# Performance work log

Hardware: AMD Instinct MI355X
Metric: run time of the kernel (lower is better)

## Reference

```python
import jax, jax.numpy as jnp
import numpy as np
import math

THRESHOLD = 0.9
CAPACITY_FACTOR = 1.0
ALPHA = 0.01


def setup_inputs() -> dict:
    key = jax.random.key(0)
    k1, k2 = jax.random.split(key)
    B, T, H, E = 8, 4096, 1024, 64
    x = jax.random.normal(k1, (B, T, H), dtype=jnp.float32)
    # kaiming-uniform-ish gate init: bound = 1/sqrt(H)
    gate_w = jax.random.uniform(k2, (E, H), dtype=jnp.float32,
                                minval=-1.0 / math.sqrt(H), maxval=1.0 / math.sqrt(H))
    return {"x": x, "gate_w": gate_w}


def reference(x, gate_w):
    B, T, H = x.shape
    E = gate_w.shape[0]
    N = B * T
    x_flat = x.reshape(N, H)

    logits = x_flat @ gate_w.T                      # [N, E]
    probs = jax.nn.softmax(logits, axis=-1)

    # per-token descending sort of expert probs
    idx_sorted = jnp.argsort(-probs, axis=-1)       # [N, E]
    p_sorted = jnp.take_along_axis(probs, idx_sorted, axis=-1)

    # variable-k threshold selection on cumulative prob
    csum = jnp.cumsum(p_sorted, axis=-1)
    reached = csum >= THRESHOLD
    reached = reached.at[:, -1].set(True)
    k_idx = jnp.argmax(reached, axis=-1)            # first True per row
    arangeE = jnp.arange(E)[None, :]
    assign_sorted = arangeE <= k_idx[:, None]       # prefix-select in sorted order

    # scatter back to expert order via inverse permutation
    inv_perm = jnp.argsort(idx_sorted, axis=-1)
    assign_mask = jnp.take_along_axis(assign_sorted, inv_perm, axis=-1)

    # priority score R: prob minus rank, -1e9 for unassigned
    rank = jnp.arange(1, E + 1, dtype=probs.dtype)[None, :]
    R_sorted = jnp.where(assign_sorted, p_sorted - rank, jnp.float32(-1e9))
    R = jnp.take_along_axis(R_sorted, inv_perm, axis=-1)  # [N, E]

    # capacity-based dropping: keep top-C tokens per expert column
    capacity = int(math.ceil(N / E) * CAPACITY_FACTOR)
    C = min(capacity, N)
    tok_sorted = jnp.argsort(-R, axis=0)            # [N, E]
    topC_tok = tok_sorted[:C, :]                    # [C, E]
    cols = jnp.broadcast_to(jnp.arange(E)[None, :], topC_tok.shape)
    keep_flags = jnp.zeros((N, E), dtype=bool).at[topC_tok, cols].set(True)

    final_mask = assign_mask & keep_flags
    scores_sel = jnp.where(final_mask, probs, jnp.zeros_like(probs))

    # aux load-balance loss on top-1 assignments
    top1_idx = jnp.argmax(probs, axis=-1)
    top1_scores = jnp.max(probs, axis=-1)
    fi = jnp.mean(jax.nn.one_hot(top1_idx, E, dtype=probs.dtype), axis=0)
    pi = jax.ops.segment_sum(top1_scores, top1_idx, num_segments=E) / jnp.float32(N)
    aux_loss = E * jnp.sum(fi * pi) * ALPHA

    return final_mask, scores_sel, aux_loss, top1_idx
```

## Files before the change

### kernel.cpp

```cpp
#include <hip/hip_runtime.h>
#include <math.h>

#define NTOK 32768
#define HDIM 1024
#define NEXP 64
#define NE   (NTOK * NEXP)
#define CAP  512
#define TB   64
#define CK   64
#define XRS  68
#define CAND 6144
#define QMAX 2048

__device__ __forceinline__ unsigned f2key(float f) {
  unsigned u = __float_as_uint(f);
  return (u & 0x80000000u) ? ~u : (u | 0x80000000u);
}
__device__ __forceinline__ int bin_of(unsigned k) {
  if (k & 0x80000000u) return 0;
  float f = __uint_as_float(~k);
  f = fminf(f, 64.5f);
  return (int)f;
}

__global__ void init_kernel(unsigned* cnt, float* sumP, unsigned* ghist) {
  int i = blockIdx.x * 256 + threadIdx.x;
  if (i < NEXP) { cnt[i] = 0u; sumP[i] = 0.f; }
  if (i < NEXP * NEXP) ghist[i] = 0u;
}

__global__ __launch_bounds__(512) void router_kernel(
    const float* __restrict__ x, const float* __restrict__ w,
    float* __restrict__ probs, unsigned* __restrict__ keyNE,
    unsigned* __restrict__ keyEN, unsigned long long* __restrict__ assignB,
    unsigned* __restrict__ cnt, float* __restrict__ sumP,
    unsigned* __restrict__ ghist, float* __restrict__ out) {
  __shared__ float sm[(TB + NEXP) * XRS];
  __shared__ unsigned lhist[NEXP * 65];
  const int tid  = threadIdx.x;
  const int wid  = tid >> 6, lane = tid & 63;
  const int tokv = wid >> 1, expv = wid & 1;
  const int tg   = lane >> 3, eg = lane & 7;
  const int t0   = blockIdx.x * TB;
  float* xs  = sm;
  float* wsm = sm + TB * XRS;

  for (int i = tid; i < NEXP * 65; i += 512) lhist[i] = 0u;

  float acc[2][4] = {};

  for (int hc = 0; hc < HDIM / CK; ++hc) {
    const int h0 = hc * CK;
#pragma unroll
    for (int r = 0; r < 2; ++r) {
      int idx = tid + r * 512;
      int row = idx >> 4, c4 = idx & 15;
      *(float4*)(xs + row * XRS + c4 * 4) =
          *(const float4*)(x + (size_t)(t0 + row) * HDIM + h0 + c4 * 4);
      *(float4*)(wsm + row * XRS + c4 * 4) =
          *(const float4*)(w + (size_t)row * HDIM + h0 + c4 * 4);
    }
    __syncthreads();
#pragma unroll
    for (int s = 0; s < 16; ++s) {
      const int k4 = s * 4;
      float4 xv0 = *(const float4*)(xs + (tokv * 16 + tg) * XRS + k4);
      float4 xv1 = *(const float4*)(xs + (tokv * 16 + 8 + tg) * XRS + k4);
#pragma unroll
      for (int j = 0; j < 4; ++j) {
        float4 wv = *(const float4*)(wsm + (expv * 32 + j * 8 + eg) * XRS + k4);
        acc[0][j] += xv0.x * wv.x + xv0.y * wv.y + xv0.z * wv.z + xv0.w * wv.w;
        acc[1][j] += xv1.x * wv.x + xv1.y * wv.y + xv1.z * wv.z + xv1.w * wv.w;
      }
    }
    __syncthreads();
  }

  float* ls = sm;
  unsigned* kt = (unsigned*)(sm + TB * 65);
#pragma unroll
  for (int i = 0; i < 2; ++i) {
    int tl = tokv * 16 + i * 8 + tg;
#pragma unroll
    for (int j = 0; j < 4; ++j)
      ls[tl * 65 + expv * 32 + j * 8 + eg] = acc[i][j];
  }
  __syncthreads();

  for (int i = 0; i < 8; ++i) {
    const int tl = wid * 8 + i;
    const int t  = t0 + tl;
    float l = ls[tl * 65 + lane];
    float mx = l;
#pragma unroll
    for (int m = 32; m >= 1; m >>= 1) mx = fmaxf(mx, __shfl_xor(mx, m));
    float ex = expf(l - mx);
    float ssum = ex;
#pragma unroll
    for (int m = 32; m >= 1; m >>= 1) ssum += __shfl_xor(ssum, m);
    float p = ex / ssum;
    int rank = 0; float csum = p;
#pragma unroll
    for (int d = 1; d < 64; ++d) {
      float pj = __shfl_xor(p, d);
      int H = d; H |= H >> 1; H |= H >> 2; H |= H >> 4; H -= (H >> 1);
      bool jlt = (lane & H) != 0;
      bool gt = (pj > p) || (pj == p && jlt);
      rank += gt ? 1 : 0;
      csum += gt ? pj : 0.f;
    }
    int kc = (csum >= 0.9f) ? rank : 63;
#pragma unroll
    for (int m = 32; m >= 1; m >>= 1) kc = min(kc, __shfl_xor(kc, m));
    const bool assign = (rank <= kc);
    float R = assign ? (p - (float)(rank + 1)) : -1e9f;
    unsigned key = f2key(R);
    probs[(size_t)t * NEXP + lane] = p;
    keyNE[(size_t)t * NEXP + lane] = key;
    kt[tl * 65 + lane] = key;
    atomicAdd(&lhist[lane * 65 + bin_of(key)], 1u);
    unsigned long long ab = __ballot(assign);
    if (lane == 0) assignB[t] = ab;
    if (rank == 0) {
      out[(size_t)2 * NE + 1 + t] = (float)lane;
      atomicAdd(&cnt[lane], 1u);
      atomicAdd(&sumP[lane], p);
    }
  }
  __syncthreads();
#pragma unroll
  for (int r = 0; r < 8; ++r) {
    int idx = tid + r * 512;
    int e = idx >> 6, tl = idx & 63;
    keyEN[(size_t)e * NTOK + t0 + tl] = kt[tl * 65 + e];
  }
  for (int idx = tid; idx < NEXP * NEXP; idx += 512) {
    int ee = idx >> 6, b = idx & 63;
    unsigned v = lhist[ee * 65 + b];
    if (v) atomicAdd(&ghist[idx], v);
  }
}

__global__ __launch_bounds__(1024) void select_kernel(
    const unsigned* __restrict__ keyEN, const unsigned* __restrict__ ghist,
    unsigned* __restrict__ theta, int* __restrict__ tieCut) {
  const int e = blockIdx.x;
  const unsigned* col = keyEN + (size_t)e * NTOK;
  const int tid = threadIdx.x, wid = tid >> 6;
  __shared__ unsigned wh[16][256];
  __shared__ unsigned h[256];
  __shared__ unsigned cA_k[CAND], cA_t[CAND], cB_k[CAND], cB_t[CAND];
  __shared__ unsigned s_n, s_b;
  __shared__ int s_rb, s_need, s_cnt;
  __shared__ unsigned s_theta; __shared__ int s_cut;

  if (tid == 0) {
    unsigned run = 0; int rb = -1, need = 0, cc = 0;
    for (int r = 0; r < 64; ++r) {
      unsigned c = ghist[e * 64 + r];
      if (rb < 0 && run + c >= CAP) { rb = r; need = CAP - (int)run; cc = (int)c; }
      run += c;
    }
    s_rb = rb; s_need = need; s_cnt = cc;
  }
  __syncthreads();
  if (s_rb < 0) {
    if (tid == 0) { theta[e] = f2key(-1e9f); tieCut[e] = -1; }
    return;
  }
  const int rb = s_rb;
  int need = s_need, cnt = s_cnt;
  unsigned pmask = 0u, pval = 0u;
  int level = 0;

  while (cnt > CAND && level < 4) {
    const int sh = 24 - 8 * level;
    for (int r = tid; r < 16 * 256; r += 1024) ((unsigned*)wh)[r] = 0u;
    __syncthreads();
    for (int t = tid; t < NTOK; t += 1024) {
      unsigned k = col[t];
      if (bin_of(k) == rb && (k & pmask) == pval)
        atomicAdd(&wh[wid][(k >> sh) & 255u], 1u);
    }
    __syncthreads();
    if (tid < 256) {
      unsigned s = 0;
      for (int wv = 0; wv < 16; ++wv) s += wh[wv][tid];
      h[tid] = s;
    }
    __syncthreads();
    if (tid == 0) {
      unsigned cum = 0;
      for (int d = 255; d >= 0; --d) {
        if (cum + h[d] >= (unsigned)need) {
          s_b = (unsigned)d; s_need = need - (int)cum; s_cnt = (int)h[d];
          break;
        }
        cum += h[d];
      }
    }
    __syncthreads();
    need = s_need; cnt = s_cnt;
    pmask |= (255u << sh); pval |= (s_b << sh);
    level++;
    __syncthreads();
  }

  if (cnt > CAND) {
    int lo = 0, hi = NTOK - 1;
    while (lo < hi) {
      int mid = (lo + hi) >> 1;
      if (tid == 0) s_n = 0u;
      __syncthreads();
      for (int t = tid; t <= mid; t += 1024)
        if (col[t] == pval) atomicAdd(&s_n, 1u);
      __syncthreads();
      if ((int)s_n >= need) hi = mid; else lo = mid + 1;
      __syncthreads();
    }
    if (tid == 0) { theta[e] = pval; tieCut[e] = lo; }
    return;
  }

  if (tid == 0) s_n = 0u;
  __syncthreads();
  for (int t = tid; t < NTOK; t += 1024) {
    unsigned k = col[t];
    if (bin_of(k) == rb && (k & pmask) == pval) {
      unsigned i = atomicAdd(&s_n, 1u);
      cA_k[i] = k; cA_t[i] = (unsigned)t;
    }
  }
  __syncthreads();
  unsigned* ck = cA_k; unsigned* ct = cA_t;
  unsigned* nk = cB_k; unsigned* nt2 = cB_t;

  while (cnt > QMAX && level < 4) {
    const int sh = 24 - 8 * level;
    for (int r = tid; r < 16 * 256; r += 1024) ((unsigned*)wh)[r] = 0u;
    __syncthreads();
    for (int i = tid; i < cnt; i += 1024)
      atomicAdd(&wh[wid][(ck[i] >> sh) & 255u], 1u);
    __syncthreads();
    if (tid < 256) {
      unsigned s = 0;
      for (int wv = 0; wv < 16; ++wv) s += wh[wv][tid];
      h[tid] = s;
    }
    __syncthreads();
    if (tid == 0) {
      unsigned cum = 0;
      for (int d = 255; d >= 0; --d) {
        if (cum + h[d] >= (unsigned)need) {
          s_b = (unsigned)d; s_need = need - (int)cum; s_cnt = (int)h[d];
          break;
        }
        cum += h[d];
      }
      s_n = 0u;
    }
    __syncthreads();
    for (int i = tid; i < cnt; i += 1024) {
      if (((ck[i] >> sh) & 255u) == s_b) {
        unsigned j = atomicAdd(&s_n, 1u);
        nk[j] = ck[i]; nt2[j] = ct[i];
      }
    }
    __syncthreads();
    { unsigned* t1 = ck; ck = nk; nk = t1; t1 = ct; ct = nt2; nt2 = t1; }
    need = s_need; cnt = s_cnt; level++;
    __syncthreads();
  }

  for (int i = tid; i < cnt; i += 1024) {
    unsigned ki = ck[i], ti = ct[i];
    int c = 0;
    for (int j = 0; j < cnt; ++j) {
      unsigned kj = ck[j], tj = ct[j];
      c += (kj > ki || (kj == ki && tj < ti)) ? 1 : 0;
    }
    if (c == need - 1) { s_theta = ki; s_cut = (int)ti; }
  }
  __syncthreads();
  if (tid == 0) { theta[e] = s_theta; tieCut[e] = s_cut; }
}

__global__ __launch_bounds__(256) void write_kernel(
    const float* __restrict__ probs, const unsigned* __restrict__ keyNE,
    const unsigned long long* __restrict__ assignB,
    const unsigned* __restrict__ theta, const int* __restrict__ tieCut,
    const unsigned* __restrict__ cnt, const float* __restrict__ sumP,
    float* __restrict__ out) {
  const int id = blockIdx.x * 256 + threadIdx.x;
  const int t = id >> 6, e = id & 63;
  unsigned k = keyNE[id];
  float p = probs[id];
  bool a = (assignB[t] >> e) & 1ull;
  unsigned th = theta[e];
  int cut = tieCut[e];
  bool keep = (k > th) || ((k == th) && (t <= cut));
  bool msk = a && keep;
  out[id] = msk ? 1.f : 0.f;
  out[(size_t)NE + id] = msk ? p : 0.f;
  if (blockIdx.x == 0 && threadIdx.x < 64) {
    int ee = threadIdx.x;
    float v = ((float)cnt[ee] / (float)NTOK) * (sumP[ee] / (float)NTOK);
#pragma unroll
    for (int m = 32; m >= 1; m >>= 1) v += __shfl_xor(v, m);
    if (ee == 0) out[(size_t)2 * NE] = (float)NEXP * v * 0.01f;
  }
}

extern "C" void kernel_launch(void* const* d_in, const int* in_sizes, int n_in,
                              void* d_out, int out_size, void* d_ws, size_t ws_size,
                              hipStream_t stream) {
  const float* x = (const float*)d_in[0];
  const float* w = (const float*)d_in[1];
  float* out = (float*)d_out;

  char* ws = (char*)d_ws;
  float* probs                 = (float*)ws;
  unsigned* keyNE              = (unsigned*)(probs + NE);
  unsigned* keyEN              = keyNE + NE;
  unsigned long long* assignB  = (unsigned long long*)(keyEN + NE);
  unsigned* cnt                = (unsigned*)(assignB + NTOK);
  float* sumP                  = (float*)(cnt + NEXP);
  unsigned* theta              = (unsigned*)(sumP + NEXP);
  int* tieCut                  = (int*)(theta + NEXP);
  unsigned* ghist              = (unsigned*)(tieCut + NEXP);

  init_kernel<<<16, 256, 0, stream>>>(cnt, sumP, ghist);
  router_kernel<<<NTOK / TB, 512, 0, stream>>>(x, w, probs, keyNE, keyEN,
                                               assignB, cnt, sumP, ghist, out);
  select_kernel<<<NEXP, 1024, 0, stream>>>(keyEN, ghist, theta, tieCut);
  write_kernel<<<NE / 256, 256, 0, stream>>>(probs, keyNE, assignB, theta,
                                             tieCut, cnt, sumP, out);
}
```

Baseline: 543.0 us.

## Restructure router GEMM: per-lane token rows, split-K across waves, register prefetch

Changes the gate GEMM so each lane owns one token and keeps all 64 expert accumulators in registers. Each wave handles a 32-wide slice of every 256-wide K chunk, reading the gate weights straight from global memory with wave-uniform addresses, so they are broadcast and cached instead of staged in LDS. x tiles are staged through XOR-swizzled shared memory, and the next chunk is prefetched into registers. Partial sums from the eight waves are reduced serially in shared memory. This trades high register pressure and a serialized 8-phase reduction for fewer LDS loads and barriers per FMA.

```diff
diff --git a/kernel.cpp b/kernel.cpp
--- a/kernel.cpp
+++ b/kernel.cpp
@@ -7,8 +7,7 @@
 #define NE   (NTOK * NEXP)
 #define CAP  512
 #define TB   64
-#define CK   64
-#define XRS  68
+#define KC   256
 #define CAND 6144
 #define QMAX 2048
 
@@ -35,62 +34,77 @@
     unsigned* __restrict__ keyEN, unsigned long long* __restrict__ assignB,
     unsigned* __restrict__ cnt, float* __restrict__ sumP,
     unsigned* __restrict__ ghist, float* __restrict__ out) {
-  __shared__ float sm[(TB + NEXP) * XRS];
-  __shared__ unsigned lhist[NEXP * 65];
+  __shared__ float4 smem4[4096];
+  char* smemb      = (char*)smem4;
+  float* lsf       = (float*)smem4;
+  unsigned* kt     = (unsigned*)smem4 + 4160;
+  unsigned* lhist  = (unsigned*)smem4 + 8320;
+
   const int tid  = threadIdx.x;
   const int wid  = tid >> 6, lane = tid & 63;
-  const int tokv = wid >> 1, expv = wid & 1;
-  const int tg   = lane >> 3, eg = lane & 7;
+  const int uw   = __builtin_amdgcn_readfirstlane(wid);
   const int t0   = blockIdx.x * TB;
-  float* xs  = sm;
-  float* wsm = sm + TB * XRS;
-
-  for (int i = tid; i < NEXP * 65; i += 512) lhist[i] = 0u;
-
-  float acc[2][4] = {};
-
-  for (int hc = 0; hc < HDIM / CK; ++hc) {
-    const int h0 = hc * CK;
-#pragma unroll
-    for (int r = 0; r < 2; ++r) {
-      int idx = tid + r * 512;
-      int row = idx >> 4, c4 = idx & 15;
-      *(float4*)(xs + row * XRS + c4 * 4) =
-          *(const float4*)(x + (size_t)(t0 + row) * HDIM + h0 + c4 * 4);
-      *(float4*)(wsm + row * XRS + c4 * 4) =
-          *(const float4*)(w + (size_t)row * HDIM + h0 + c4 * 4);
-    }
-    __syncthreads();
-#pragma unroll
-    for (int s = 0; s < 16; ++s) {
-      const int k4 = s * 4;
-      float4 xv0 = *(const float4*)(xs + (tokv * 16 + tg) * XRS + k4);
-      float4 xv1 = *(const float4*)(xs + (tokv * 16 + 8 + tg) * XRS + k4);
-#pragma unroll
-      for (int j = 0; j < 4; ++j) {
-        float4 wv = *(const float4*)(wsm + (expv * 32 + j * 8 + eg) * XRS + k4);
-        acc[0][j] += xv0.x * wv.x + xv0.y * wv.y + xv0.z * wv.z + xv0.w * wv.w;
-        acc[1][j] += xv1.x * wv.x + xv1.y * wv.y + xv1.z * wv.z + xv1.w * wv.w;
+  const int swz  = (lane & 7) << 4;
+
+  float acc[64];
+#pragma unroll
+  for (int e = 0; e < 64; ++e) acc[e] = 0.f;
+
+  float4 stg[8];
+#pragma unroll
+  for (int rr = 0; rr < 8; ++rr)
+    stg[rr] = *(const float4*)(x + (size_t)(t0 + uw * 8 + rr) * HDIM + lane * 4);
+
+#pragma unroll 1
+  for (int c = 0; c < HDIM / KC; ++c) {
+    const int c0 = c * KC;
+#pragma unroll
+    for (int rr = 0; rr < 8; ++rr) {
+      const int row = uw * 8 + rr;
+      *(float4*)(smemb + row * 1024 + ((lane * 16) ^ ((row & 7) << 4))) = stg[rr];
+    }
+    __syncthreads();
+    float4 xr[8];
+#pragma unroll
+    for (int s = 0; s < 8; ++s)
+      xr[s] = *(const float4*)(smemb + lane * 1024 + (((uw * 8 + s) * 16) ^ swz));
+    if (c < HDIM / KC - 1) {
+#pragma unroll
+      for (int rr = 0; rr < 8; ++rr)
+        stg[rr] = *(const float4*)(x + (size_t)(t0 + uw * 8 + rr) * HDIM +
+                                   (c0 + KC) + lane * 4);
+    }
+    const int kb = c0 + uw * 32;
+#pragma unroll
+    for (int e = 0; e < 64; ++e) {
+      const float* wp = w + (size_t)e * HDIM + kb;
+#pragma unroll
+      for (int s = 0; s < 8; ++s) {
+        float4 wv = *(const float4*)(wp + s * 4);
+        acc[e] = fmaf(xr[s].x, wv.x, acc[e]);
+        acc[e] = fmaf(xr[s].y, wv.y, acc[e]);
+        acc[e] = fmaf(xr[s].z, wv.z, acc[e]);
+        acc[e] = fmaf(xr[s].w, wv.w, acc[e]);
       }
     }
     __syncthreads();
   }
 
-  float* ls = sm;
-  unsigned* kt = (unsigned*)(sm + TB * 65);
-#pragma unroll
-  for (int i = 0; i < 2; ++i) {
-    int tl = tokv * 16 + i * 8 + tg;
-#pragma unroll
-    for (int j = 0; j < 4; ++j)
-      ls[tl * 65 + expv * 32 + j * 8 + eg] = acc[i][j];
-  }
-  __syncthreads();
+  for (int i = tid; i < 64 * 65; i += 512) { lsf[i] = 0.f; lhist[i] = 0u; }
+  __syncthreads();
+#pragma unroll 1
+  for (int ph = 0; ph < 8; ++ph) {
+    if (wid == ph) {
+#pragma unroll
+      for (int e = 0; e < 64; ++e) lsf[lane * 65 + e] += acc[e];
+    }
+    __syncthreads();
+  }
 
   for (int i = 0; i < 8; ++i) {
     const int tl = wid * 8 + i;
     const int t  = t0 + tl;
-    float l = ls[tl * 65 + lane];
+    float l = lsf[tl * 65 + lane];
     float mx = l;
 #pragma unroll
     for (int m = 32; m >= 1; m >>= 1) mx = fmaxf(mx, __shfl_xor(mx, m));
```

After: 748.5 us. 37.9% more time.
